# Kernel tuning notes

Hardware: AMD Instinct MI355X
Metric: run time of the kernel (lower is better)

## Reference

```python
import jax, jax.numpy as jnp
import numpy as np

INPUT_DIM = 3072
D_MODEL = 128      # mamba_hidden_dim
EXPAND = 2
D_INNER = EXPAND * D_MODEL   # 256
D_STATE = 16
D_CONV = 4
DT_RANK = D_MODEL // 16      # 8
NUM_LANES = 6
B, L = 4, 2048


def rmsnorm(x, w, eps=1e-5):
    return x * jax.lax.rsqrt(jnp.mean(x * x, axis=-1, keepdims=True) + eps) * w


def mamba_block(x, W_in, conv_w, conv_b, W_x, W_dt, b_dt, A_log, Dp, W_out):
    # x: [B, L, D_MODEL]
    bsz, seqlen, _ = x.shape
    xz = x @ W_in                              # [B, L, 2*D_INNER]
    xs, res = jnp.split(xz, 2, axis=-1)        # each [B, L, D_INNER]

    # depthwise causal conv1d over time
    xc = jnp.transpose(xs, (0, 2, 1))          # [B, C, L]
    k = conv_w[:, None, :]                     # [C, 1, K]
    xc = jax.lax.conv_general_dilated(
        xc, k, window_strides=(1,), padding=[(D_CONV - 1, 0)],
        dimension_numbers=('NCH', 'OIH', 'NCH'), feature_group_count=D_INNER)
    xc = xc + conv_b[None, :, None]
    xs = jax.nn.silu(jnp.transpose(xc, (0, 2, 1)))  # [B, L, C]

    # input-dependent SSM parameters
    dbl = xs @ W_x                             # [B, L, DT_RANK + 2*D_STATE]
    dt = dbl[..., :DT_RANK]
    Bm = dbl[..., DT_RANK:DT_RANK + D_STATE]   # [B, L, S]
    Cm = dbl[..., DT_RANK + D_STATE:]          # [B, L, S]
    delta = jax.nn.softplus(dt @ W_dt + b_dt)  # [B, L, C]

    A = -jnp.exp(A_log)                        # [C, S]
    dA = jnp.exp(delta[..., None] * A)                           # [B, L, C, S]
    dBu = delta[..., None] * Bm[:, :, None, :] * xs[..., None]   # [B, L, C, S]

    def step(h, inp):
        dA_t, dBu_t, C_t = inp                 # [B,C,S], [B,C,S], [B,S]
        h = dA_t * h + dBu_t
        y = jnp.einsum('bcs,bs->bc', h, C_t)
        return h, y

    h0 = jnp.zeros((bsz, D_INNER, D_STATE), x.dtype)
    _, ys = jax.lax.scan(
        step, h0,
        (jnp.moveaxis(dA, 1, 0), jnp.moveaxis(dBu, 1, 0), jnp.moveaxis(Cm, 1, 0)))
    y = jnp.moveaxis(ys, 0, 1) + xs * Dp       # [B, L, C]
    y = y * jax.nn.silu(res)
    return y @ W_out                           # [B, L, D_MODEL]


def setup_inputs() -> dict:
    key = jax.random.key(0)
    ks = jax.random.split(key, 12)
    s = 0.02
    inp = {
        'x': jax.random.normal(ks[0], (B, L, INPUT_DIM), jnp.float32),
        'W_emb': jax.random.normal(ks[1], (INPUT_DIM, D_MODEL), jnp.float32) * s,
        'b_emb': jnp.zeros((D_MODEL,), jnp.float32),
        'norm_w': jnp.ones((D_MODEL,), jnp.float32),
        'W_in': jax.random.normal(ks[2], (D_MODEL, 2 * D_INNER), jnp.float32) * s,
        'conv_w': jax.random.normal(ks[3], (D_INNER, D_CONV), jnp.float32) * 0.1,
        'conv_b': jnp.zeros((D_INNER,), jnp.float32),
        'W_x': jax.random.normal(ks[4], (D_INNER, DT_RANK + 2 * D_STATE), jnp.float32) * s,
        'W_dt': jax.random.normal(ks[5], (DT_RANK, D_INNER), jnp.float32) * s,
        'b_dt': jnp.full((D_INNER,), -2.0, jnp.float32),
        'A_log': jnp.log(jnp.broadcast_to(jnp.arange(1, D_STATE + 1, dtype=jnp.float32), (D_INNER, D_STATE))),
        'Dp': jnp.ones((D_INNER,), jnp.float32),
        'W_out': jax.random.normal(ks[6], (D_INNER, D_MODEL), jnp.float32) * s,
        'normf_w': jnp.ones((D_MODEL,), jnp.float32),
        'W_head': jax.random.normal(ks[7], (D_MODEL, NUM_LANES), jnp.float32) * s,
        'b_head': jnp.zeros((NUM_LANES,), jnp.float32),
    }
    return inp


def reference(x, W_emb, b_emb, norm_w, W_in, conv_w, conv_b, W_x, W_dt, b_dt,
              A_log, Dp, W_out, normf_w, W_head, b_head):
    h = x @ W_emb + b_emb                        # project 3072 -> 128
    h = h + mamba_block(rmsnorm(h, norm_w), W_in, conv_w, conv_b, W_x, W_dt,
                        b_dt, A_log, Dp, W_out)  # residual Mamba block
    Fm = rmsnorm(h, normf_w)
    # dropout is identity in eval
    out = Fm @ W_head + b_head                   # [B, L, NUM_LANES]
    pi = jax.nn.softmax(out, axis=-1)
    lane_preds = jnp.argmax(pi, axis=-1)
    return pi, lane_preds
```

## Files before the change

kernel.cpp:

```cpp
#include <hip/hip_runtime.h>
#include <hip/hip_bf16.h>
#include <math.h>

constexpr int B_ = 4, L_ = 2048, IN_DIM = 3072, DM = 128, DI = 256, DS = 16, NL = 6;
constexpr int ROWS = B_ * L_;
constexpr int SPLITK = 8, KC = IN_DIM / SPLITK;

typedef __attribute__((ext_vector_type(8))) short short8b;
typedef __attribute__((ext_vector_type(4))) float f32x4;

static __device__ __forceinline__ float silu_f(float x) {
  return x / (1.f + __expf(-x));
}

static __device__ __forceinline__ unsigned short f2bf_rne(float v) {
  unsigned u = __float_as_uint(v);
  unsigned r = u + 0x7FFFu + ((u >> 16) & 1u);
  return (unsigned short)(r >> 16);
}

__global__ __launch_bounds__(256) void wsplit_kernel(const float* __restrict__ W,
                                                     unsigned short* __restrict__ wt_hi,
                                                     unsigned short* __restrict__ wt_lo) {
  int tid = threadIdx.x;
  int c = tid & 127;
  int kc = blockIdx.x * 16 + (tid >> 7) * 8;
  short8b vh, vl;
#pragma unroll
  for (int j = 0; j < 8; ++j) {
    float v = W[(size_t)(kc + j) * DM + c];
    unsigned short h = f2bf_rne(v);
    float hf = __uint_as_float((unsigned)h << 16);
    vh[j] = (short)h;
    vl[j] = (short)f2bf_rne(v - hf);
  }
  *(short8b*)&wt_hi[(size_t)c * IN_DIM + kc] = vh;
  *(short8b*)&wt_lo[(size_t)c * IN_DIM + kc] = vl;
}

__global__ __launch_bounds__(256) void gemm_emb_mfma(const float* __restrict__ A,
                                                     const unsigned short* __restrict__ wt_hi,
                                                     const unsigned short* __restrict__ wt_lo,
                                                     float* __restrict__ part) {
  constexpr int BM = 64, BK = 32, LDA = 40;
  __shared__ unsigned short Ah[BM][LDA], Al[BM][LDA];
  __shared__ unsigned short Bh[DM][LDA], Bl[DM][LDA];
  int split = blockIdx.x;
  int bm = blockIdx.y * BM;
  int kb = split * KC;
  int tid = threadIdx.x;
  int w = tid >> 6, l = tid & 63;
  int fr = l & 15, fk = (l >> 4) * 8;

  f32x4 acc[8] = {};

  for (int k0 = 0; k0 < KC; k0 += BK) {
    {
      int r = tid >> 2, kq = (tid & 3) * 8;
      const float* src = &A[(size_t)(bm + r) * IN_DIM + kb + k0 + kq];
      float4 v0 = *(const float4*)src;
      float4 v1 = *(const float4*)(src + 4);
      float vv[8] = {v0.x, v0.y, v0.z, v0.w, v1.x, v1.y, v1.z, v1.w};
      short8b vh, vl;
#pragma unroll
      for (int j = 0; j < 8; ++j) {
        unsigned short h = f2bf_rne(vv[j]);
        float hf = __uint_as_float((unsigned)h << 16);
        vh[j] = (short)h;
        vl[j] = (short)f2bf_rne(vv[j] - hf);
      }
      *(short8b*)&Ah[r][kq] = vh;
      *(short8b*)&Al[r][kq] = vl;
    }
    {
      int c = tid >> 1, kq = (tid & 1) * 16;
      const unsigned short* sh = &wt_hi[(size_t)c * IN_DIM + kb + k0 + kq];
      const unsigned short* sl = &wt_lo[(size_t)c * IN_DIM + kb + k0 + kq];
      *(short8b*)&Bh[c][kq] = *(const short8b*)sh;
      *(short8b*)&Bh[c][kq + 8] = *(const short8b*)(sh + 8);
      *(short8b*)&Bl[c][kq] = *(const short8b*)sl;
      *(short8b*)&Bl[c][kq + 8] = *(const short8b*)(sl + 8);
    }
    __syncthreads();
    short8b ah = *(short8b*)&Ah[16 * w + fr][fk];
    short8b al = *(short8b*)&Al[16 * w + fr][fk];
#pragma unroll
    for (int t = 0; t < 8; ++t) {
      short8b bh = *(short8b*)&Bh[16 * t + fr][fk];
      short8b bl = *(short8b*)&Bl[16 * t + fr][fk];
      acc[t] = __builtin_amdgcn_mfma_f32_16x16x32_bf16(ah, bh, acc[t], 0, 0, 0);
      acc[t] = __builtin_amdgcn_mfma_f32_16x16x32_bf16(ah, bl, acc[t], 0, 0, 0);
      acc[t] = __builtin_amdgcn_mfma_f32_16x16x32_bf16(al, bh, acc[t], 0, 0, 0);
    }
    __syncthreads();
  }
  int orow = bm + 16 * w + (l >> 4) * 4;
#pragma unroll
  for (int t = 0; t < 8; ++t) {
#pragma unroll
    for (int r = 0; r < 4; ++r) {
      part[((size_t)split * ROWS + orow + r) * DM + 16 * t + fr] = acc[t][r];
    }
  }
}

__global__ __launch_bounds__(256) void reduce_rms_kernel(const float* __restrict__ part,
                                                         const float* __restrict__ b_emb,
                                                         const float* __restrict__ norm_w,
                                                         float* __restrict__ h0,
                                                         float* __restrict__ u) {
  int wave = threadIdx.x >> 6, lane = threadIdx.x & 63;
  int row = blockIdx.x * 4 + wave;
  float sx = 0.f, sy = 0.f;
#pragma unroll
  for (int sp = 0; sp < SPLITK; ++sp) {
    float2 v = *(const float2*)(part + ((size_t)sp * ROWS + row) * DM + 2 * lane);
    sx += v.x;
    sy += v.y;
  }
  float2 be = *(const float2*)(b_emb + 2 * lane);
  sx += be.x;
  sy += be.y;
  float2 hv = {sx, sy};
  *(float2*)(h0 + (size_t)row * DM + 2 * lane) = hv;
  float ss = sx * sx + sy * sy;
#pragma unroll
  for (int o = 32; o >= 1; o >>= 1) ss += __shfl_xor(ss, o);
  float rs = 1.f / sqrtf(ss * (1.f / 128.f) + 1e-5f);
  float2 wv = *(const float2*)(norm_w + 2 * lane);
  float2 o2 = {sx * rs * wv.x, sy * rs * wv.y};
  *(float2*)(u + (size_t)row * DM + 2 * lane) = o2;
}

__global__ __launch_bounds__(256) void gemm_in(const float* __restrict__ A,
                                               const float* __restrict__ Bv,
                                               float* __restrict__ C) {
  constexpr int BM = 64, BK = 32, N = 512;
  __shared__ float As[BK][BM + 4];
  __shared__ float Bs[BK][128 + 4];
  int bn = blockIdx.x * 128;
  int bm = blockIdx.y * BM;
  int tid = threadIdx.x;
  int tm = tid >> 4, tn = tid & 15;
  float acc[4][8] = {};
  for (int k0 = 0; k0 < DM; k0 += BK) {
#pragma unroll
    for (int p = 0; p < 2; ++p) {
      int i = tid + p * 256;
      int r = i >> 3, kq = (i & 7) * 4;
      float4 a4 = *(const float4*)&A[(size_t)(bm + r) * DM + k0 + kq];
      As[kq + 0][r] = a4.x;
      As[kq + 1][r] = a4.y;
      As[kq + 2][r] = a4.z;
      As[kq + 3][r] = a4.w;
    }
#pragma unroll
    for (int p = 0; p < 4; ++p) {
      int i = tid + p * 256;
      int r = i >> 5, c = (i & 31) * 4;
      *(float4*)&Bs[r][c] = *(const float4*)&Bv[(size_t)(k0 + r) * N + bn + c];
    }
    __syncthreads();
#pragma unroll
    for (int kk = 0; kk < BK; ++kk) {
      float4 a4 = *(const float4*)&As[kk][tm * 4];
      float4 b0 = *(const float4*)&Bs[kk][tn * 4];
      float4 b1 = *(const float4*)&Bs[kk][64 + tn * 4];
      float a[4] = {a4.x, a4.y, a4.z, a4.w};
      float b[8] = {b0.x, b0.y, b0.z, b0.w, b1.x, b1.y, b1.z, b1.w};
#pragma unroll
      for (int i = 0; i < 4; ++i)
#pragma unroll
        for (int j = 0; j < 8; ++j) acc[i][j] = fmaf(a[i], b[j], acc[i][j]);
    }
    __syncthreads();
  }
#pragma unroll
  for (int i = 0; i < 4; ++i) {
    size_t rowoff = (size_t)(bm + tm * 4 + i) * N + bn;
    float4 o0 = {acc[i][0], acc[i][1], acc[i][2], acc[i][3]};
    float4 o1 = {acc[i][4], acc[i][5], acc[i][6], acc[i][7]};
    *(float4*)&C[rowoff + tn * 4] = o0;
    *(float4*)&C[rowoff + 64 + tn * 4] = o1;
  }
}

__global__ __launch_bounds__(256) void conv_silu_kernel(const float* __restrict__ xz,
                                                        const float* __restrict__ conv_w,
                                                        const float* __restrict__ conv_b,
                                                        float* __restrict__ xs_row,
                                                        float* __restrict__ xs_T) {
  __shared__ float tile[64][65];
  __shared__ float cw[64][4];
  __shared__ float cb[64];
  int b = blockIdx.z, l0 = blockIdx.y * 64, c0 = blockIdx.x * 64;
  int tid = threadIdx.x;
  cw[tid / 4][tid % 4] = conv_w[(size_t)c0 * 4 + tid];
  if (tid < 64) cb[tid] = conv_b[c0 + tid];
  __syncthreads();
  int cl = tid % 64;
  int lbase = tid / 64;
#pragma unroll
  for (int i = 0; i < 16; ++i) {
    int ll = lbase + 4 * i;
    int l = l0 + ll;
    float acc = cb[cl];
#pragma unroll
    for (int k = 0; k < 4; ++k) {
      int li = l + k - 3;
      if (li >= 0) acc = fmaf(xz[((size_t)(b * L_ + li)) * 512 + c0 + cl], cw[cl][k], acc);
    }
    tile[ll][cl] = silu_f(acc);
  }
  __syncthreads();
  for (int i = tid; i < 4096; i += 256) {
    int lr = i / 64, c = i % 64;
    xs_row[((size_t)(b * L_ + l0 + lr)) * DI + c0 + c] = tile[lr][c];
  }
  for (int i = tid; i < 4096; i += 256) {
    int c = i / 64, lr = i % 64;
    xs_T[((size_t)(b * DI + c0 + c)) * L_ + l0 + lr] = tile[lr][c];
  }
}

__global__ __launch_bounds__(256) void dbl_kernel(const float* __restrict__ xs_row,
                                                  const float* __restrict__ W_x,
                                                  float* __restrict__ dbl) {
  __shared__ float Xs[32][257];
  __shared__ float Wx[256 * 40];
  int tid = threadIdx.x;
  int r0 = blockIdx.x * 32;
  for (int i = tid; i < 32 * 64; i += 256) {
    int r = i >> 6, kq = (i & 63) * 4;
    float4 v = *(const float4*)&xs_row[(size_t)(r0 + r) * DI + kq];
    Xs[r][kq + 0] = v.x;
    Xs[r][kq + 1] = v.y;
    Xs[r][kq + 2] = v.z;
    Xs[r][kq + 3] = v.w;
  }
  for (int i = tid; i < 256 * 40; i += 256) Wx[i] = W_x[i];
  __syncthreads();
  int r = tid & 31, q = tid >> 5;
  float acc[5] = {};
  for (int k = 0; k < 256; ++k) {
    float v = Xs[r][k];
#pragma unroll
    for (int j = 0; j < 5; ++j) acc[j] = fmaf(v, Wx[k * 40 + q * 5 + j], acc[j]);
  }
#pragma unroll
  for (int j = 0; j < 5; ++j) dbl[(size_t)(r0 + r) * 40 + q * 5 + j] = acc[j];
}

__global__ __launch_bounds__(256) void delta_kernel(const float* __restrict__ dbl,
                                                    const float* __restrict__ W_dt,
                                                    const float* __restrict__ b_dt,
                                                    float* __restrict__ delta_T) {
  __shared__ float Tile[32][257];
  __shared__ float Dt[32][8];
  __shared__ float Wdt[8 * 256];
  int tid = threadIdx.x;
  int r0 = blockIdx.x * 32;
  int b = r0 / L_, l0 = r0 % L_;
  if (tid < 256) {
    int r = tid >> 3, k = tid & 7;
    Dt[r][k] = dbl[(size_t)(r0 + r) * 40 + k];
  }
  for (int i = tid; i < 8 * 256; i += 256) Wdt[i] = W_dt[i];
  __syncthreads();
  int c = tid;
  float bd = b_dt[c];
  for (int r = 0; r < 32; ++r) {
    float a = bd;
#pragma unroll
    for (int k = 0; k < 8; ++k) a = fmaf(Dt[r][k], Wdt[k * 256 + c], a);
    Tile[r][c] = (a > 20.f) ? a : log1pf(__expf(a));
  }
  __syncthreads();
  for (int i = tid; i < 32 * 256; i += 256) {
    int cc = i >> 5, rr = i & 31;
    delta_T[((size_t)(b * DI + cc)) * L_ + l0 + rr] = Tile[rr][cc];
  }
}

__global__ __launch_bounds__(512) void scan_kernel(const float* __restrict__ delta_T,
                                                   const float* __restrict__ xs_T,
                                                   const float* __restrict__ dbl,
                                                   const float* __restrict__ A_log,
                                                   const float* __restrict__ Dp,
                                                   const float* __restrict__ xz,
                                                   float* __restrict__ y) {
  __shared__ float s_aprod[32][16];
  __shared__ float s_hend[32][16];
  __shared__ float s_hstart[32][16];
  int tid = threadIdx.x;
  int k = tid >> 4, s = tid & 15;
  int g = blockIdx.x;
  int b = g >> 8, c = g & 255;
  float A = -__expf(A_log[c * DS + s]);
  float dpc = Dp[c];
  const float* dp = delta_T + (size_t)g * L_ + k * 64;
  const float* xp = xs_T + (size_t)g * L_ + k * 64;
  const float* bp = dbl + ((size_t)(b * L_ + k * 64)) * 40 + 8 + s;
  const float* cp = dbl + ((size_t)(b * L_ + k * 64)) * 40 + 24 + s;

  float aprod = 1.f, h = 0.f;
  for (int j = 0; j < 64; j += 4) {
    float4 d4 = *(const float4*)(dp + j);
    float4 x4 = *(const float4*)(xp + j);
    float dj[4] = {d4.x, d4.y, d4.z, d4.w};
    float xj[4] = {x4.x, x4.y, x4.z, x4.w};
#pragma unroll
    for (int u = 0; u < 4; ++u) {
      float Bv = bp[(size_t)(j + u) * 40];
      float dA = __expf(dj[u] * A);
      aprod *= dA;
      h = fmaf(dA, h, dj[u] * Bv * xj[u]);
    }
  }
  s_aprod[k][s] = aprod;
  s_hend[k][s] = h;
  __syncthreads();

  if (tid < 16) {
    float hh = 0.f;
    for (int kk = 0; kk < 32; ++kk) {
      s_hstart[kk][tid] = hh;
      hh = fmaf(s_aprod[kk][tid], hh, s_hend[kk][tid]);
    }
  }
  __syncthreads();

  h = s_hstart[k][s];
  float* yp = y + ((size_t)(b * L_) + k * 64) * DI + c;
  const float* rp = xz + ((size_t)(b * L_) + k * 64) * 512 + 256 + c;
  for (int j = 0; j < 64; j += 4) {
    float4 d4 = *(const float4*)(dp + j);
    float4 x4 = *(const float4*)(xp + j);
    float dj[4] = {d4.x, d4.y, d4.z, d4.w};
    float xj[4] = {x4.x, x4.y, x4.z, x4.w};
#pragma unroll
    for (int u = 0; u < 4; ++u) {
      float Bv = bp[(size_t)(j + u) * 40];
      float Cv = cp[(size_t)(j + u) * 40];
      float dA = __expf(dj[u] * A);
      h = fmaf(dA, h, dj[u] * Bv * xj[u]);
      float p = h * Cv;
      p += __shfl_xor(p, 8, 16);
      p += __shfl_xor(p, 4, 16);
      p += __shfl_xor(p, 2, 16);
      p += __shfl_xor(p, 1, 16);
      if (s == 0) {
        float res = rp[(size_t)(j + u) * 512];
        yp[(size_t)(j + u) * DI] = (p + xj[u] * dpc) * silu_f(res);
      }
    }
  }
}

__global__ __launch_bounds__(256) void final_gemm_kernel(const float* __restrict__ y,
                                                         const float* __restrict__ W_out,
                                                         const float* __restrict__ h0,
                                                         const float* __restrict__ normf_w,
                                                         const float* __restrict__ W_head,
                                                         const float* __restrict__ b_head,
                                                         float* __restrict__ pi_out,
                                                         float* __restrict__ pred_out) {
  constexpr int BM = 32, BK = 32;
  __shared__ float As[BK][BM + 4];
  __shared__ float Bs[BK][128 + 4];
  __shared__ float Wh[128 * 6];
  int tid = threadIdx.x;
  int tm = tid >> 4, tn = tid & 15;
  int bm = blockIdx.x * BM;
  for (int i = tid; i < 768; i += 256) Wh[i] = W_head[i];
  float acc[2][8] = {};
  for (int k0 = 0; k0 < DI; k0 += BK) {
    {
      int r = tid >> 3, kq = (tid & 7) * 4;
      float4 a4 = *(const float4*)&y[(size_t)(bm + r) * DI + k0 + kq];
      As[kq + 0][r] = a4.x;
      As[kq + 1][r] = a4.y;
      As[kq + 2][r] = a4.z;
      As[kq + 3][r] = a4.w;
    }
#pragma unroll
    for (int p = 0; p < 4; ++p) {
      int i = tid + p * 256;
      int r = i >> 5, c = (i & 31) * 4;
      *(float4*)&Bs[r][c] = *(const float4*)&W_out[(size_t)(k0 + r) * DM + c];
    }
    __syncthreads();
#pragma unroll
    for (int kk = 0; kk < BK; ++kk) {
      float a0 = As[kk][tm * 2], a1 = As[kk][tm * 2 + 1];
      float4 b0 = *(const float4*)&Bs[kk][tn * 4];
      float4 b1 = *(const float4*)&Bs[kk][64 + tn * 4];
      float b[8] = {b0.x, b0.y, b0.z, b0.w, b1.x, b1.y, b1.z, b1.w};
#pragma unroll
      for (int j = 0; j < 8; ++j) acc[0][j] = fmaf(a0, b[j], acc[0][j]);
#pragma unroll
      for (int j = 0; j < 8; ++j) acc[1][j] = fmaf(a1, b[j], acc[1][j]);
    }
    __syncthreads();
  }
  float4 nwa = *(const float4*)&normf_w[tn * 4];
  float4 nwb = *(const float4*)&normf_w[64 + tn * 4];
  float nw[8] = {nwa.x, nwa.y, nwa.z, nwa.w, nwb.x, nwb.y, nwb.z, nwb.w};
  float bh[6];
#pragma unroll
  for (int j = 0; j < 6; ++j) bh[j] = b_head[j];
#pragma unroll
  for (int i = 0; i < 2; ++i) {
    int row = bm + tm * 2 + i;
    float4 h0a = *(const float4*)&h0[(size_t)row * DM + tn * 4];
    float4 h0b = *(const float4*)&h0[(size_t)row * DM + 64 + tn * 4];
    float hv[8] = {acc[i][0] + h0a.x, acc[i][1] + h0a.y, acc[i][2] + h0a.z, acc[i][3] + h0a.w,
                   acc[i][4] + h0b.x, acc[i][5] + h0b.y, acc[i][6] + h0b.z, acc[i][7] + h0b.w};
    float ss = 0.f;
#pragma unroll
    for (int j = 0; j < 8; ++j) ss += hv[j] * hv[j];
    ss += __shfl_xor(ss, 1);
    ss += __shfl_xor(ss, 2);
    ss += __shfl_xor(ss, 4);
    ss += __shfl_xor(ss, 8);
    float rs = 1.f / sqrtf(ss * (1.f / 128.f) + 1e-5f);
    float lg[6] = {};
#pragma unroll
    for (int j = 0; j < 8; ++j) {
      float fm = hv[j] * rs * nw[j];
      int col = (j < 4) ? (tn * 4 + j) : (64 + tn * 4 + (j - 4));
#pragma unroll
      for (int l = 0; l < 6; ++l) lg[l] = fmaf(fm, Wh[col * 6 + l], lg[l]);
    }
#pragma unroll
    for (int l = 0; l < 6; ++l) {
      lg[l] += __shfl_xor(lg[l], 1);
      lg[l] += __shfl_xor(lg[l], 2);
      lg[l] += __shfl_xor(lg[l], 4);
      lg[l] += __shfl_xor(lg[l], 8);
      lg[l] += bh[l];
    }
    if (tn == 0) {
      float mv = lg[0];
      int am = 0;
#pragma unroll
      for (int l = 1; l < 6; ++l)
        if (lg[l] > mv) { mv = lg[l]; am = l; }
      float e[6], sum = 0.f;
#pragma unroll
      for (int l = 0; l < 6; ++l) { e[l] = __expf(lg[l] - mv); sum += e[l]; }
      float inv = 1.f / sum;
#pragma unroll
      for (int l = 0; l < 6; ++l) pi_out[(size_t)row * NL + l] = e[l] * inv;
      pred_out[row] = (float)am;
    }
  }
}

extern "C" void kernel_launch(void* const* d_in, const int* in_sizes, int n_in,
                              void* d_out, int out_size, void* d_ws, size_t ws_size,
                              hipStream_t stream) {
  const float* x = (const float*)d_in[0];
  const float* W_emb = (const float*)d_in[1];
  const float* b_emb = (const float*)d_in[2];
  const float* norm_w = (const float*)d_in[3];
  const float* W_in = (const float*)d_in[4];
  const float* conv_w = (const float*)d_in[5];
  const float* conv_b = (const float*)d_in[6];
  const float* W_x = (const float*)d_in[7];
  const float* W_dt = (const float*)d_in[8];
  const float* b_dt = (const float*)d_in[9];
  const float* A_log = (const float*)d_in[10];
  const float* Dp = (const float*)d_in[11];
  const float* W_out = (const float*)d_in[12];
  const float* normf_w = (const float*)d_in[13];
  const float* W_head = (const float*)d_in[14];
  const float* b_head = (const float*)d_in[15];

  float* ws = (float*)d_ws;
  float* h0 = ws;
  float* u = h0 + 1048576;
  float* xz = u + 1048576;
  float* xs_row = xz + 4194304;
  float* xs_T = xs_row + 2097152;
  float* dbl = xs_T + 2097152;
  float* delta_T = dbl + 327680;
  float* y = delta_T + 2097152;

  float* part = xz;
  unsigned short* wt_hi = (unsigned short*)delta_T;
  unsigned short* wt_lo = wt_hi + (size_t)IN_DIM * DM;

  float* pi_out = (float*)d_out;
  float* pred_out = pi_out + (size_t)ROWS * NL;

  wsplit_kernel<<<192, 256, 0, stream>>>(W_emb, wt_hi, wt_lo);
  gemm_emb_mfma<<<dim3(SPLITK, ROWS / 64), 256, 0, stream>>>(x, wt_hi, wt_lo, part);
  reduce_rms_kernel<<<ROWS / 4, 256, 0, stream>>>(part, b_emb, norm_w, h0, u);
  gemm_in<<<dim3(4, 128), 256, 0, stream>>>(u, W_in, xz);
  conv_silu_kernel<<<dim3(4, 32, 4), 256, 0, stream>>>(xz, conv_w, conv_b, xs_row, xs_T);
  dbl_kernel<<<256, 256, 0, stream>>>(xs_row, W_x, dbl);
  delta_kernel<<<256, 256, 0, stream>>>(dbl, W_dt, b_dt, delta_T);
  scan_kernel<<<1024, 512, 0, stream>>>(delta_T, xs_T, dbl, A_log, Dp, xz, y);
  final_gemm_kernel<<<256, 256, 0, stream>>>(y, W_out, h0, normf_w, W_head, b_head, pi_out, pred_out);
}
```

Baseline: 377.5 us.

## Transpose gate branch to channel-major and write scan output in place as float4

The conv kernel gets extra blocks that transpose the res half of xz into a channel-major buffer. The scan kernel then reads res with contiguous float4 loads and overwrites that same buffer with y using float4 stores, instead of doing strided scalar reads and writes with a stride of 512 or 256 floats. The final GEMM reads y in channel-major order, so its A-tile load becomes a direct float4 copy. The cost is an extra transpose pass over 8 MB of res data, and the in-place aliasing drops the restrict qualifier.

```diff
diff --git a/kernel.cpp b/kernel.cpp
--- a/kernel.cpp
+++ b/kernel.cpp
@@ -189,37 +189,54 @@
                                                         const float* __restrict__ conv_w,
                                                         const float* __restrict__ conv_b,
                                                         float* __restrict__ xs_row,
-                                                        float* __restrict__ xs_T) {
+                                                        float* __restrict__ xs_T,
+                                                        float* __restrict__ res_T) {
   __shared__ float tile[64][65];
   __shared__ float cw[64][4];
   __shared__ float cb[64];
-  int b = blockIdx.z, l0 = blockIdx.y * 64, c0 = blockIdx.x * 64;
-  int tid = threadIdx.x;
-  cw[tid / 4][tid % 4] = conv_w[(size_t)c0 * 4 + tid];
-  if (tid < 64) cb[tid] = conv_b[c0 + tid];
-  __syncthreads();
+  int cx = blockIdx.x;
+  int b = blockIdx.z, l0 = blockIdx.y * 64;
+  int tid = threadIdx.x;
   int cl = tid % 64;
   int lbase = tid / 64;
-#pragma unroll
-  for (int i = 0; i < 16; ++i) {
-    int ll = lbase + 4 * i;
-    int l = l0 + ll;
-    float acc = cb[cl];
-#pragma unroll
-    for (int k = 0; k < 4; ++k) {
-      int li = l + k - 3;
-      if (li >= 0) acc = fmaf(xz[((size_t)(b * L_ + li)) * 512 + c0 + cl], cw[cl][k], acc);
-    }
-    tile[ll][cl] = silu_f(acc);
-  }
-  __syncthreads();
-  for (int i = tid; i < 4096; i += 256) {
-    int lr = i / 64, c = i % 64;
-    xs_row[((size_t)(b * L_ + l0 + lr)) * DI + c0 + c] = tile[lr][c];
-  }
-  for (int i = tid; i < 4096; i += 256) {
-    int c = i / 64, lr = i % 64;
-    xs_T[((size_t)(b * DI + c0 + c)) * L_ + l0 + lr] = tile[lr][c];
+  if (cx < 4) {
+    int c0 = cx * 64;
+    cw[tid / 4][tid % 4] = conv_w[(size_t)c0 * 4 + tid];
+    if (tid < 64) cb[tid] = conv_b[c0 + tid];
+    __syncthreads();
+#pragma unroll
+    for (int i = 0; i < 16; ++i) {
+      int ll = lbase + 4 * i;
+      int l = l0 + ll;
+      float acc = cb[cl];
+#pragma unroll
+      for (int k = 0; k < 4; ++k) {
+        int li = l + k - 3;
+        if (li >= 0) acc = fmaf(xz[((size_t)(b * L_ + li)) * 512 + c0 + cl], cw[cl][k], acc);
+      }
+      tile[ll][cl] = silu_f(acc);
+    }
+    __syncthreads();
+    for (int i = tid; i < 4096; i += 256) {
+      int lr = i / 64, c = i % 64;
+      xs_row[((size_t)(b * L_ + l0 + lr)) * DI + c0 + c] = tile[lr][c];
+    }
+    for (int i = tid; i < 4096; i += 256) {
+      int c = i / 64, lr = i % 64;
+      xs_T[((size_t)(b * DI + c0 + c)) * L_ + l0 + lr] = tile[lr][c];
+    }
+  } else {
+    int c0 = (cx - 4) * 64;
+#pragma unroll
+    for (int i = 0; i < 16; ++i) {
+      int ll = lbase + 4 * i;
+      tile[ll][cl] = xz[((size_t)(b * L_ + l0 + ll)) * 512 + 256 + c0 + cl];
+    }
+    __syncthreads();
+    for (int i = tid; i < 4096; i += 256) {
+      int c = i / 64, lr = i % 64;
+      res_T[((size_t)(b * DI + c0 + c)) * L_ + l0 + lr] = tile[lr][c];
+    }
   }
 }
 
@@ -287,8 +304,7 @@
                                                    const float* __restrict__ dbl,
                                                    const float* __restrict__ A_log,
                                                    const float* __restrict__ Dp,
-                                                   const float* __restrict__ xz,
-                                                   float* __restrict__ y) {
+                                                   float* resy) {
   __shared__ float s_aprod[32][16];
   __shared__ float s_hend[32][16];
   __shared__ float s_hstart[32][16];
@@ -331,13 +347,15 @@
   __syncthreads();
 
   h = s_hstart[k][s];
-  float* yp = y + ((size_t)(b * L_) + k * 64) * DI + c;
-  const float* rp = xz + ((size_t)(b * L_) + k * 64) * 512 + 256 + c;
+  float* rp = resy + (size_t)g * L_ + k * 64;
   for (int j = 0; j < 64; j += 4) {
     float4 d4 = *(const float4*)(dp + j);
     float4 x4 = *(const float4*)(xp + j);
+    float4 r4 = *(const float4*)(rp + j);
     float dj[4] = {d4.x, d4.y, d4.z, d4.w};
     float xj[4] = {x4.x, x4.y, x4.z, x4.w};
+    float rj[4] = {r4.x, r4.y, r4.z, r4.w};
+    float p4[4];
 #pragma unroll
     for (int u = 0; u < 4; ++u) {
       float Bv = bp[(size_t)(j + u) * 40];
@@ -349,15 +367,16 @@
       p += __shfl_xor(p, 4, 16);
       p += __shfl_xor(p, 2, 16);
       p += __shfl_xor(p, 1, 16);
-      if (s == 0) {
-        float res = rp[(size_t)(j + u) * 512];
-        yp[(size_t)(j + u) * DI] = (p + xj[u] * dpc) * silu_f(res);
-      }
-    }
-  }
-}
-
-__global__ __launch_bounds__(256) void final_gemm_kernel(const float* __restrict__ y,
+      p4[u] = (p + xj[u] * dpc) * silu_f(rj[u]);
+    }
+    if (s == 0) {
+      float4 o = {p4[0], p4[1], p4[2], p4[3]};
+      *(float4*)(rp + j) = o;
+    }
+  }
+}
+
+__global__ __launch_bounds__(256) void final_gemm_kernel(const float* __restrict__ yT,
                                                          const float* __restrict__ W_out,
                                                          const float* __restrict__ h0,
                                                          const float* __restrict__ normf_w,
@@ -372,16 +391,14 @@
   int tid = threadIdx.x;
   int tm = tid >> 4, tn = tid & 15;
   int bm = blockIdx.x * BM;
+  int b = bm >> 11, l0 = bm & (L_ - 1);
   for (int i = tid; i < 768; i += 256) Wh[i] = W_head[i];
   float acc[2][8] = {};
   for (int k0 = 0; k0 < DI; k0 += BK) {
     {
-      int r = tid >> 3, kq = (tid & 7) * 4;
-      float4 a4 = *(const float4*)&y[(size_t)(bm + r) * DI + k0 + kq];
-      As[kq + 0][r] = a4.x;
-      As[kq + 1][r] = a4.y;
-      As[kq + 2][r] = a4.z;
-      As[kq + 3][r] = a4.w;
+      int cc = tid >> 3, lq = (tid & 7) * 4;
+      float4 v = *(const float4*)&yT[((size_t)(b * DI + k0 + cc)) * L_ + l0 + lq];
+      *(float4*)&As[cc][lq] = v;
     }
 #pragma unroll
     for (int p = 0; p < 4; ++p) {
@@ -395,11 +412,11 @@
       float a0 = As[kk][tm * 2], a1 = As[kk][tm * 2 + 1];
       float4 b0 = *(const float4*)&Bs[kk][tn * 4];
       float4 b1 = *(const float4*)&Bs[kk][64 + tn * 4];
-      float b[8] = {b0.x, b0.y, b0.z, b0.w, b1.x, b1.y, b1.z, b1.w};
-#pragma unroll
-      for (int j = 0; j < 8; ++j) acc[0][j] = fmaf(a0, b[j], acc[0][j]);
-#pragma unroll
-      for (int j = 0; j < 8; ++j) acc[1][j] = fmaf(a1, b[j], acc[1][j]);
+      float bb[8] = {b0.x, b0.y, b0.z, b0.w, b1.x, b1.y, b1.z, b1.w};
+#pragma unroll
+      for (int j = 0; j < 8; ++j) acc[0][j] = fmaf(a0, bb[j], acc[0][j]);
+#pragma unroll
+      for (int j = 0; j < 8; ++j) acc[1][j] = fmaf(a1, bb[j], acc[1][j]);
     }
     __syncthreads();
   }
@@ -485,7 +502,7 @@
   float* xs_T = xs_row + 2097152;
   float* dbl = xs_T + 2097152;
   float* delta_T = dbl + 327680;
-  float* y = delta_T + 2097152;
+  float* resy = delta_T + 2097152;
 
   float* part = xz;
   unsigned short* wt_hi = (unsigned short*)delta_T;
@@ -498,9 +515,9 @@
   gemm_emb_mfma<<<dim3(SPLITK, ROWS / 64), 256, 0, stream>>>(x, wt_hi, wt_lo, part);
   reduce_rms_kernel<<<ROWS / 4, 256, 0, stream>>>(part, b_emb, norm_w, h0, u);
   gemm_in<<<dim3(4, 128), 256, 0, stream>>>(u, W_in, xz);
-  conv_silu_kernel<<<dim3(4, 32, 4), 256, 0, stream>>>(xz, conv_w, conv_b, xs_row, xs_T);
+  conv_silu_kernel<<<dim3(8, 32, 4), 256, 0, stream>>>(xz, conv_w, conv_b, xs_row, xs_T, resy);
   dbl_kernel<<<256, 256, 0, stream>>>(xs_row, W_x, dbl);
   delta_kernel<<<256, 256, 0, stream>>>(dbl, W_dt, b_dt, delta_T);
-  scan_kernel<<<1024, 512, 0, stream>>>(delta_T, xs_T, dbl, A_log, Dp, xz, y);
-  final_gemm_kernel<<<256, 256, 0, stream>>>(y, W_out, h0, normf_w, W_head, b_head, pi_out, pred_out);
-}
+  scan_kernel<<<1024, 512, 0, stream>>>(delta_T, xs_T, dbl, A_log, Dp, resy);
+  final_gemm_kernel<<<256, 256, 0, stream>>>(resy, W_out, h0, normf_w, W_head, b_head, pi_out, pred_out);
+}
```

After: 357.9 us. 1.05x faster.
